# Performance work log

Hardware: AMD Instinct MI355X
Metric: run time of the kernel (lower is better)

## Reference

```python
import jax, jax.numpy as jnp
import numpy as np

N, IN_DIM, EMB = 65536, 768, 128
CB_SIZES = [8, 64, 512]
COMMIT = 0.25  # standard EMA-VQ commitment cost


def setup_inputs() -> dict:
    key = jax.random.key(0)
    ks = jax.random.split(key, 12)
    s = 0.02
    return {
        "x": jax.random.normal(ks[0], (N, IN_DIM), jnp.float32),
        "W_e1": jax.random.normal(ks[1], (IN_DIM, IN_DIM), jnp.float32) * s,
        "b_e1": jnp.zeros((IN_DIM,), jnp.float32),
        "W_e2": jax.random.normal(ks[2], (EMB, IN_DIM), jnp.float32) * s,
        "b_e2": jnp.zeros((EMB,), jnp.float32),
        "W_d1": jax.random.normal(ks[3], (EMB, EMB), jnp.float32) * s,
        "b_d1": jnp.zeros((EMB,), jnp.float32),
        "W_d2": jax.random.normal(ks[4], (EMB, EMB), jnp.float32) * s,
        "b_d2": jnp.zeros((EMB,), jnp.float32),
        "E0": jax.random.normal(ks[5], (CB_SIZES[0], EMB), jnp.float32),
        "E1": jax.random.normal(ks[6], (CB_SIZES[1], EMB), jnp.float32),
        "E2": jax.random.normal(ks[7], (CB_SIZES[2], EMB), jnp.float32),
    }


def _quantize(r, E):
    # squared L2 distances [N, K] = |r|^2 - 2 r.E^T + |E|^2
    d = (jnp.sum(r * r, axis=-1, keepdims=True)
         - 2.0 * jnp.einsum("nd,kd->nk", r, E)
         + jnp.sum(E * E, axis=-1))
    idx = jnp.argmin(d, axis=-1)          # [N]
    z_q = E[idx]                           # gather [N, EMB]
    loss = COMMIT * jnp.mean((jax.lax.stop_gradient(z_q) - r) ** 2)
    z_q_st = r + jax.lax.stop_gradient(z_q - r)  # straight-through
    return z_q_st, loss, idx


def reference(x, W_e1, b_e1, W_e2, b_e2, W_d1, b_d1, W_d2, b_d2, E0, E1, E2):
    # encoder MLP
    h = jax.nn.relu(x @ W_e1.T + b_e1)
    z = h @ W_e2.T + b_e2                 # [N, EMB]

    residual = z
    quantized_sum = jnp.zeros_like(z)
    total_loss = jnp.float32(0.0)
    all_indices = []
    for E in (E0, E1, E2):                # fixed depth=3 residual VQ loop
        z_q, loss, idx = _quantize(residual, E)
        residual = residual - z_q
        quantized_sum = quantized_sum + z_q
        total_loss = total_loss + loss
        all_indices.append(idx)

    # decoder MLP
    h2 = jax.nn.relu(quantized_sum @ W_d1.T + b_d1)
    reconstructed = h2 @ W_d2.T + b_d2    # [N, EMB]
    codes = jnp.stack(all_indices, axis=1)  # [N, depth]
    return reconstructed, total_loss, codes
```

## Files before the change

### kernel.cpp

```cpp
#include <hip/hip_runtime.h>

typedef _Float16 f16;
typedef __attribute__((ext_vector_type(4))) _Float16 f16x4;
typedef __attribute__((ext_vector_type(8))) _Float16 f16x8;
typedef __attribute__((ext_vector_type(4))) float    f32x4;

static constexpr int NROWS = 65536;
static constexpr int D_IN  = 768;
static constexpr int D_EMB = 128;
static constexpr long LOSS_OFF  = (long)NROWS * D_EMB;
static constexpr long CODES_OFF = LOSS_OFF + 1;

static constexpr long WOFF = 201326592L;
static constexpr long WE1H = 0,       WE1L = 589824;
static constexpr long WE2H = 1179648, WE2L = 1277952;
static constexpr long WD1F = 1376256, WD2F = 1392640;
static constexpr long PARTIAL_B = WOFF + 4194304L;

__device__ __forceinline__ float dot4(float4 a, float4 b){
  return fmaf(a.x,b.x, fmaf(a.y,b.y, fmaf(a.z,b.z, a.w*b.w)));
}

__device__ __forceinline__ void split4(float4 v, f16x4& hi, f16x4& lo){
  _Float16 h0=(_Float16)v.x, h1=(_Float16)v.y, h2=(_Float16)v.z, h3=(_Float16)v.w;
  hi[0]=h0; hi[1]=h1; hi[2]=h2; hi[3]=h3;
  lo[0]=(_Float16)((v.x-(float)h0)*2048.0f);
  lo[1]=(_Float16)((v.y-(float)h1)*2048.0f);
  lo[2]=(_Float16)((v.z-(float)h2)*2048.0f);
  lo[3]=(_Float16)((v.w-(float)h3)*2048.0f);
}

__device__ __forceinline__ void split8_reg(const float* v, f16x8& hi, f16x8& lo){
#pragma unroll
  for (int i = 0; i < 8; i++){
    _Float16 h = (_Float16)v[i];
    hi[i] = h;
    lo[i] = (_Float16)((v[i]-(float)h)*2048.0f);
  }
}

__global__ __launch_bounds__(256)
void split_weights_kernel(const float* __restrict__ We1, const float* __restrict__ We2,
                          const float* __restrict__ Wd1, const float* __restrict__ Wd2,
                          f16* __restrict__ wp){
  int t = blockIdx.x*256 + threadIdx.x;
  if (t >= 180224) return;
  if (t < 147456){
    long o4 = t; float4 v = *(const float4*)(We1 + o4*4);
    f16x4 h4, l4; split4(v, h4, l4);
    *(f16x4*)(wp + WE1H + o4*4) = h4; *(f16x4*)(wp + WE1L + o4*4) = l4;
  } else if (t < 172032){
    long o4 = t - 147456; float4 v = *(const float4*)(We2 + o4*4);
    f16x4 h4, l4; split4(v, h4, l4);
    *(f16x4*)(wp + WE2H + o4*4) = h4; *(f16x4*)(wp + WE2L + o4*4) = l4;
  } else if (t < 176128){
    long o4 = t - 172032; float4 v = *(const float4*)(Wd1 + o4*4);
    f16x4 h4; h4[0]=(_Float16)v.x; h4[1]=(_Float16)v.y; h4[2]=(_Float16)v.z; h4[3]=(_Float16)v.w;
    *(f16x4*)(wp + WD1F + o4*4) = h4;
  } else {
    long o4 = t - 176128; float4 v = *(const float4*)(Wd2 + o4*4);
    f16x4 h4; h4[0]=(_Float16)v.x; h4[1]=(_Float16)v.y; h4[2]=(_Float16)v.z; h4[3]=(_Float16)v.w;
    *(f16x4*)(wp + WD2F + o4*4) = h4;
  }
}

template<bool RELU>
__global__ __launch_bounds__(256, 2)
void gemm_mfma_kernel(const float* __restrict__ A, const float* __restrict__ B,
                      const float* __restrict__ bias, float* __restrict__ C,
                      int M, int N, int K) {
  constexpr int RS = 40;
  __shared__ f16 Ah[128*RS];
  __shared__ f16 Al[128*RS];
  __shared__ f16 Bhs[128*RS];
  __shared__ f16 Bls[128*RS];

  const int tid  = threadIdx.x;
  const int wave = tid >> 6, lane = tid & 63;
  const int wm = wave >> 1, wn = wave & 1;
  const int lr = lane & 15, lg = lane >> 4;
  const long m0 = (long)blockIdx.y * 128;
  const long n0 = (long)blockIdx.x * 128;
  const float* Ab = A + m0 * K;
  const float* Bb = B + n0 * K;
  const int srow = tid >> 3;
  const int sc4  = tid & 7;

  float4 pa[4], pb[4];
#pragma unroll
  for (int p = 0; p < 4; p++){
    pa[p] = *(const float4*)(Ab + (long)(p*32 + srow)*K + sc4*4);
    pb[p] = *(const float4*)(Bb + (long)(p*32 + srow)*K + sc4*4);
  }

  f32x4 accm[4][4], accc[4][4];
#pragma unroll
  for (int i = 0; i < 4; i++)
#pragma unroll
    for (int j = 0; j < 4; j++){
      accm[i][j] = (f32x4){0.f,0.f,0.f,0.f};
      accc[i][j] = (f32x4){0.f,0.f,0.f,0.f};
    }

  const int nt = K / 32;
  for (int t = 0; t < nt; t++){
    __syncthreads();
#pragma unroll
    for (int p = 0; p < 4; p++){
      int r = p*32 + srow;
      f16x4 h4, l4;
      split4(pa[p], h4, l4);
      *(f16x4*)&Ah[r*RS + sc4*4] = h4;
      *(f16x4*)&Al[r*RS + sc4*4] = l4;
      split4(pb[p], h4, l4);
      *(f16x4*)&Bhs[r*RS + sc4*4] = h4;
      *(f16x4*)&Bls[r*RS + sc4*4] = l4;
    }
    __syncthreads();
    if (t + 1 < nt){
      const float* An = Ab + (t+1)*32;
      const float* Bn = Bb + (t+1)*32;
#pragma unroll
      for (int p = 0; p < 4; p++){
        pa[p] = *(const float4*)(An + (long)(p*32 + srow)*K + sc4*4);
        pb[p] = *(const float4*)(Bn + (long)(p*32 + srow)*K + sc4*4);
      }
    }
    f16x8 ah[4], al[4];
#pragma unroll
    for (int mi = 0; mi < 4; mi++){
      int row = wm*64 + mi*16 + lr;
      ah[mi] = *(const f16x8*)&Ah[row*RS + lg*8];
      al[mi] = *(const f16x8*)&Al[row*RS + lg*8];
    }
#pragma unroll
    for (int ni = 0; ni < 4; ni++){
      int col = wn*64 + ni*16 + lr;
      f16x8 bh = *(const f16x8*)&Bhs[col*RS + lg*8];
      f16x8 bl = *(const f16x8*)&Bls[col*RS + lg*8];
#pragma unroll
      for (int mi = 0; mi < 4; mi++){
        accm[mi][ni] = __builtin_amdgcn_mfma_f32_16x16x32_f16(ah[mi], bh, accm[mi][ni], 0, 0, 0);
        accc[mi][ni] = __builtin_amdgcn_mfma_f32_16x16x32_f16(ah[mi], bl, accc[mi][ni], 0, 0, 0);
        accc[mi][ni] = __builtin_amdgcn_mfma_f32_16x16x32_f16(al[mi], bh, accc[mi][ni], 0, 0, 0);
      }
    }
  }

  float bv[4];
#pragma unroll
  for (int ni = 0; ni < 4; ni++) bv[ni] = bias[n0 + wn*64 + ni*16 + lr];
#pragma unroll
  for (int mi = 0; mi < 4; mi++){
#pragma unroll
    for (int ni = 0; ni < 4; ni++){
#pragma unroll
      for (int r = 0; r < 4; r++){
        float v = accm[mi][ni][r] + accc[mi][ni][r]*(1.0f/2048.0f) + bv[ni];
        if (RELU) v = fmaxf(v, 0.f);
        long row = m0 + wm*64 + mi*16 + lg*4 + r;
        C[row*N + n0 + wn*64 + ni*16 + lr] = v;
      }
    }
  }
}

template<bool RELU, bool OUT16>
__global__ __launch_bounds__(256)
void gemm_f16_dec(const f16* __restrict__ Ag, const f16* __restrict__ Bg,
                  const float* __restrict__ bias,
                  float* __restrict__ C32, f16* __restrict__ C16, int M){
  constexpr int RS = 136;
  __shared__ f16 As[128*RS];
  __shared__ f16 Bs[128*RS];
  const int tid = threadIdx.x;
  const int wave = tid >> 6, lane = tid & 63;
  const int wm = wave >> 1, wn = wave & 1;
  const int lr = lane & 15, lg = lane >> 4;
  const long m0 = (long)blockIdx.y * 128;
  const int srow = tid >> 1, sco = (tid & 1) * 64;

#pragma unroll
  for (int c = 0; c < 8; c++){
    *(f16x8*)&As[srow*RS + sco + c*8] = *(const f16x8*)(Ag + (m0+srow)*128 + sco + c*8);
    *(f16x8*)&Bs[srow*RS + sco + c*8] = *(const f16x8*)(Bg + (long)srow*128 + sco + c*8);
  }
  __syncthreads();

  f32x4 acc[4][4];
#pragma unroll
  for (int i = 0; i < 4; i++)
#pragma unroll
    for (int j = 0; j < 4; j++) acc[i][j] = (f32x4){0.f,0.f,0.f,0.f};

#pragma unroll
  for (int ks = 0; ks < 4; ks++){
    f16x8 a[4];
#pragma unroll
    for (int mi = 0; mi < 4; mi++)
      a[mi] = *(const f16x8*)&As[(wm*64 + mi*16 + lr)*RS + ks*32 + lg*8];
#pragma unroll
    for (int ni = 0; ni < 4; ni++){
      f16x8 b = *(const f16x8*)&Bs[(wn*64 + ni*16 + lr)*RS + ks*32 + lg*8];
#pragma unroll
      for (int mi = 0; mi < 4; mi++)
        acc[mi][ni] = __builtin_amdgcn_mfma_f32_16x16x32_f16(a[mi], b, acc[mi][ni], 0, 0, 0);
    }
  }

  float bv[4];
#pragma unroll
  for (int ni = 0; ni < 4; ni++) bv[ni] = bias[wn*64 + ni*16 + lr];
#pragma unroll
  for (int mi = 0; mi < 4; mi++){
#pragma unroll
    for (int ni = 0; ni < 4; ni++){
#pragma unroll
      for (int r = 0; r < 4; r++){
        float v = acc[mi][ni][r] + bv[ni];
        if (RELU) v = fmaxf(v, 0.f);
        long row = m0 + wm*64 + mi*16 + lg*4 + r;
        long col = wn*64 + ni*16 + lr;
        if (OUT16) C16[row*128 + col] = (_Float16)v;
        else       C32[row*128 + col] = v;
      }
    }
  }
}

__global__ __launch_bounds__(256)
void vq_mfma_kernel(const float* __restrict__ z,
                    const float* __restrict__ E0c, const float* __restrict__ E1c,
                    const float* __restrict__ E2c,
                    f16* __restrict__ q16, float* __restrict__ out,
                    float* __restrict__ partial){
  constexpr int VS = 132;
  constexpr int ES = 136;
  __shared__ float rs[64*VS];
  __shared__ f16 Eh[64*ES];
  __shared__ f16 El[64*ES];
  __shared__ float pE[4*64];
  __shared__ int   besti[3*64];
  __shared__ float wsum[4];

  const int tid  = threadIdx.x;
  const int wave = tid >> 6, lane = tid & 63;
  const int lr = lane & 15, lg = lane >> 4;
  const int row0 = blockIdx.x * 64;
  const int urow = tid & 63, uq = tid >> 6;
  const int sc = tid & 63, sq = tid >> 6;

#pragma unroll
  for (int i = 0; i < 8; i++){
    int idx = i*256 + tid;
    int r = idx >> 5, c = (idx & 31) * 4;
    *(float4*)&rs[r*VS + c] = *(const float4*)&z[(long)(row0 + r)*D_EMB + c];
  }

  float4 qa[8];
#pragma unroll
  for (int j = 0; j < 8; j++) qa[j] = make_float4(0.f,0.f,0.f,0.f);
  float lsum = 0.f;

  const float* Etab[3] = {E0c, E1c, E2c};
  const int    Ktab[3] = {8, 64, 512};

  for (int l = 0; l < 3; l++){
    const float* E = Etab[l];
    const int K = Ktab[l];

    __syncthreads();
    f16x8 ah[4], al[4];
#pragma unroll
    for (int ks = 0; ks < 4; ks++){
      float av[8];
      *(float4*)&av[0] = *(const float4*)&rs[(wave*16 + lr)*VS + ks*32 + lg*8];
      *(float4*)&av[4] = *(const float4*)&rs[(wave*16 + lr)*VS + ks*32 + lg*8 + 4];
      split8_reg(av, ah[ks], al[ks]);
    }

    float bd[4]; int bi[4];
#pragma unroll
    for (int r = 0; r < 4; r++){ bd[r] = 3.0e38f; bi[r] = 0x7fffffff; }

    for (int kbase = 0; kbase < K; kbase += 64){
      const int cn = (K - kbase < 64) ? (K - kbase) : 64;
      __syncthreads();
      if (sc < cn){
        float s = 0.f;
#pragma unroll
        for (int j = 0; j < 8; j++){
          float4 v = *(const float4*)&E[(long)(kbase + sc)*D_EMB + sq*32 + j*4];
          s += dot4(v, v);
          f16x4 h4, l4; split4(v, h4, l4);
          *(f16x4*)&Eh[sc*ES + sq*32 + j*4] = h4;
          *(f16x4*)&El[sc*ES + sq*32 + j*4] = l4;
        }
        pE[sq*64 + sc] = s;
      } else {
        f16x4 zz; zz[0]=(_Float16)0.f; zz[1]=(_Float16)0.f; zz[2]=(_Float16)0.f; zz[3]=(_Float16)0.f;
#pragma unroll
        for (int j = 0; j < 8; j++){
          *(f16x4*)&Eh[sc*ES + sq*32 + j*4] = zz;
          *(f16x4*)&El[sc*ES + sq*32 + j*4] = zz;
        }
        pE[sq*64 + sc] = 3.0e38f;
      }
      __syncthreads();

      const int cgmax = (cn + 15) >> 4;
      for (int cg = 0; cg < cgmax; cg++){
        f32x4 Sm = (f32x4){0.f,0.f,0.f,0.f};
        f32x4 Sc = (f32x4){0.f,0.f,0.f,0.f};
#pragma unroll
        for (int ks = 0; ks < 4; ks++){
          f16x8 bh = *(const f16x8*)&Eh[(cg*16 + lr)*ES + ks*32 + lg*8];
          f16x8 bl = *(const f16x8*)&El[(cg*16 + lr)*ES + ks*32 + lg*8];
          Sm = __builtin_amdgcn_mfma_f32_16x16x32_f16(ah[ks], bh, Sm, 0, 0, 0);
          Sc = __builtin_amdgcn_mfma_f32_16x16x32_f16(ah[ks], bl, Sc, 0, 0, 0);
          Sc = __builtin_amdgcn_mfma_f32_16x16x32_f16(al[ks], bh, Sc, 0, 0, 0);
        }
        int code = cg*16 + lr;
        float ne = pE[code] + pE[64+code] + pE[128+code] + pE[192+code];
        int kg = kbase + code;
#pragma unroll
        for (int r = 0; r < 4; r++){
          float S  = fmaf(Sc[r], 1.0f/2048.0f, Sm[r]);
          float sd = fmaf(-2.0f, S, ne);
          if (sd < bd[r]){ bd[r] = sd; bi[r] = kg; }
        }
      }
    }

#pragma unroll
    for (int r = 0; r < 4; r++){
#pragma unroll
      for (int off = 1; off < 16; off <<= 1){
        float ob = __shfl_xor(bd[r], off, 16);
        int   oi = __shfl_xor(bi[r], off, 16);
        if (ob < bd[r] || (ob == bd[r] && oi < bi[r])){ bd[r] = ob; bi[r] = oi; }
      }
      if (lr == 0) besti[l*64 + wave*16 + lg*4 + r] = bi[r];
    }
    __syncthreads();

    {
      int k = besti[l*64 + urow];
      const float* Er = E + (long)k*D_EMB + uq*32;
#pragma unroll
      for (int j = 0; j < 8; j++){
        float4 e = *(const float4*)&Er[j*4];
        float* rp = &rs[urow*VS + uq*32 + j*4];
        float4 r = *(const float4*)rp;
        float4 df = make_float4(e.x-r.x, e.y-r.y, e.z-r.z, e.w-r.w);
        lsum += dot4(df, df);
        *(float4*)rp = make_float4(r.x-e.x, r.y-e.y, r.z-e.z, r.w-e.w);
        qa[j].x += e.x; qa[j].y += e.y; qa[j].z += e.z; qa[j].w += e.w;
      }
    }
  }

  __syncthreads();
#pragma unroll
  for (int j = 0; j < 8; j++)
    *(float4*)&rs[urow*VS + uq*32 + j*4] = qa[j];
  __syncthreads();
#pragma unroll
  for (int i = 0; i < 8; i++){
    int idx = i*256 + tid;
    int r = idx >> 5, c = (idx & 31) * 4;
    float4 v = *(const float4*)&rs[r*VS + c];
    f16x4 h4; h4[0]=(_Float16)v.x; h4[1]=(_Float16)v.y; h4[2]=(_Float16)v.z; h4[3]=(_Float16)v.w;
    *(f16x4*)&q16[(long)(row0 + r)*D_EMB + c] = h4;
  }
  if (tid < 64){
    long n = row0 + tid;
    for (int l = 0; l < 3; l++)
      out[CODES_OFF + n*3 + l] = (float)besti[l*64 + tid];
  }
  for (int off = 32; off > 0; off >>= 1) lsum += __shfl_down(lsum, off);
  if ((tid & 63) == 0) wsum[tid >> 6] = lsum;
  __syncthreads();
  if (tid == 0) partial[blockIdx.x] = wsum[0] + wsum[1] + wsum[2] + wsum[3];
}

__global__ __launch_bounds__(256)
void loss_reduce_kernel(const float* __restrict__ partial, float* __restrict__ out){
  __shared__ float ws2[4];
  int tid = threadIdx.x;
  float s = 0.f;
  for (int i = tid; i < 1024; i += 256) s += partial[i];
  for (int off = 32; off > 0; off >>= 1) s += __shfl_down(s, off);
  if ((tid & 63) == 0) ws2[tid >> 6] = s;
  __syncthreads();
  if (tid == 0)
    out[LOSS_OFF] = (ws2[0] + ws2[1] + ws2[2] + ws2[3]) * (0.25f / (float)((long)NROWS * D_EMB));
}

extern "C" void kernel_launch(void* const* d_in, const int* in_sizes, int n_in,
                              void* d_out, int out_size, void* d_ws, size_t ws_size,
                              hipStream_t stream) {
  (void)in_sizes; (void)n_in; (void)out_size; (void)ws_size;
  const float* x   = (const float*)d_in[0];
  const float* We1 = (const float*)d_in[1];
  const float* be1 = (const float*)d_in[2];
  const float* We2 = (const float*)d_in[3];
  const float* be2 = (const float*)d_in[4];
  const float* Wd1 = (const float*)d_in[5];
  const float* bd1 = (const float*)d_in[6];
  const float* Wd2 = (const float*)d_in[7];
  const float* bd2 = (const float*)d_in[8];
  const float* E0  = (const float*)d_in[9];
  const float* E1  = (const float*)d_in[10];
  const float* E2  = (const float*)d_in[11];
  float* out = (float*)d_out;
  char*  ws  = (char*)d_ws;

  float* h    = (float*)ws;
  f16*   q16  = (f16*)ws;
  f16*   h216 = (f16*)(ws + 33554432L);
  f16*   wp   = (f16*)(ws + WOFF);
  float* partial = (float*)(ws + PARTIAL_B);
  float* z = out;

  dim3 blk(256);
  split_weights_kernel<<<dim3(704), blk, 0, stream>>>(We1, We2, Wd1, Wd2, wp);
  gemm_mfma_kernel<true ><<<dim3(D_IN/128,  NROWS/128), blk, 0, stream>>>(x, We1, be1, h, NROWS, D_IN,  D_IN);
  gemm_mfma_kernel<false><<<dim3(D_EMB/128, NROWS/128), blk, 0, stream>>>(h, We2, be2, z, NROWS, D_EMB, D_IN);
  vq_mfma_kernel<<<dim3(NROWS/64), blk, 0, stream>>>(z, E0, E1, E2, q16, out, partial);
  loss_reduce_kernel<<<dim3(1), blk, 0, stream>>>(partial, out);
  gemm_f16_dec<true, true ><<<dim3(1, NROWS/128), blk, 0, stream>>>(q16,  wp+WD1F, bd1, nullptr, h216, NROWS);
  gemm_f16_dec<false,false><<<dim3(1, NROWS/128), blk, 0, stream>>>(h216, wp+WD2F, bd2, out, nullptr, NROWS);
}
```

Measured before the change: 516.7 us.

## Load pre-split MFMA-packed encoder weights directly from global, skip B LDS staging

The encoder weight matrices are now split into f16 hi/lo once and stored in an MFMA-fragment-packed layout, so the encoder GEMMs read B operands straight from global/L2 into registers instead of re-splitting fp32 weights into LDS every tile. This removes per-tile B conversion work and halves LDS usage, which may raise occupancy. A block-index swizzle is also added to group workgroups for better L2 locality. The risk is added global-load latency on the B path, since it is no longer prefetched a tile ahead.

```diff
diff --git a/kernel.cpp b/kernel.cpp
--- a/kernel.cpp
+++ b/kernel.cpp
@@ -12,10 +12,10 @@
 static constexpr long CODES_OFF = LOSS_OFF + 1;
 
 static constexpr long WOFF = 201326592L;
-static constexpr long WE1H = 0,       WE1L = 589824;
-static constexpr long WE2H = 1179648, WE2L = 1277952;
+static constexpr long PK1H = 0,       PK1L = 589824;
+static constexpr long PK2H = 1179648, PK2L = 1277952;
 static constexpr long WD1F = 1376256, WD2F = 1392640;
-static constexpr long PARTIAL_B = WOFF + 4194304L;
+static constexpr long PARTIAL_B = WOFF + 3145728L;
 
 __device__ __forceinline__ float dot4(float4 a, float4 b){
   return fmaf(a.x,b.x, fmaf(a.y,b.y, fmaf(a.z,b.z, a.w*b.w)));
@@ -46,13 +46,20 @@
   int t = blockIdx.x*256 + threadIdx.x;
   if (t >= 180224) return;
   if (t < 147456){
-    long o4 = t; float4 v = *(const float4*)(We1 + o4*4);
+    int n = t / 192, k0 = (t % 192) * 4;
+    float4 v = *(const float4*)(We1 + (long)n*768 + k0);
     f16x4 h4, l4; split4(v, h4, l4);
-    *(f16x4*)(wp + WE1H + o4*4) = h4; *(f16x4*)(wp + WE1L + o4*4) = l4;
+    long idx = (((long)(n>>4)*24 + (k0>>5))*64 + ((k0>>3)&3)*16 + (n&15))*8 + (k0&7);
+    *(f16x4*)(wp + PK1H + idx) = h4;
+    *(f16x4*)(wp + PK1L + idx) = l4;
   } else if (t < 172032){
-    long o4 = t - 147456; float4 v = *(const float4*)(We2 + o4*4);
+    int u = t - 147456;
+    int n = u / 192, k0 = (u % 192) * 4;
+    float4 v = *(const float4*)(We2 + (long)n*768 + k0);
     f16x4 h4, l4; split4(v, h4, l4);
-    *(f16x4*)(wp + WE2H + o4*4) = h4; *(f16x4*)(wp + WE2L + o4*4) = l4;
+    long idx = (((long)(n>>4)*24 + (k0>>5))*64 + ((k0>>3)&3)*16 + (n&15))*8 + (k0&7);
+    *(f16x4*)(wp + PK2H + idx) = h4;
+    *(f16x4*)(wp + PK2L + idx) = l4;
   } else if (t < 176128){
     long o4 = t - 172032; float4 v = *(const float4*)(Wd1 + o4*4);
     f16x4 h4; h4[0]=(_Float16)v.x; h4[1]=(_Float16)v.y; h4[2]=(_Float16)v.z; h4[3]=(_Float16)v.w;
@@ -66,32 +73,35 @@
 
 template<bool RELU>
 __global__ __launch_bounds__(256, 2)
-void gemm_mfma_kernel(const float* __restrict__ A, const float* __restrict__ B,
-                      const float* __restrict__ bias, float* __restrict__ C,
-                      int M, int N, int K) {
+void gemm_bL2_kernel(const float* __restrict__ A,
+                     const f16* __restrict__ Bph, const f16* __restrict__ Bpl,
+                     const float* __restrict__ bias, float* __restrict__ C,
+                     int M, int N, int K){
   constexpr int RS = 40;
   __shared__ f16 Ah[128*RS];
   __shared__ f16 Al[128*RS];
-  __shared__ f16 Bhs[128*RS];
-  __shared__ f16 Bls[128*RS];
-
-  const int tid  = threadIdx.x;
+
+  const int tid = threadIdx.x;
   const int wave = tid >> 6, lane = tid & 63;
   const int wm = wave >> 1, wn = wave & 1;
   const int lr = lane & 15, lg = lane >> 4;
-  const long m0 = (long)blockIdx.y * 128;
-  const long n0 = (long)blockIdx.x * 128;
+
+  const int nwg = gridDim.x * gridDim.y;
+  const int lid = blockIdx.y * gridDim.x + blockIdx.x;
+  const int sw  = (lid & 7) * (nwg >> 3) + (lid >> 3);
+  const int bx  = sw % gridDim.x, by = sw / gridDim.x;
+
+  const long m0 = (long)by * 128;
+  const long n0 = (long)bx * 128;
+  const int kcs = K >> 5;
   const float* Ab = A + m0 * K;
-  const float* Bb = B + n0 * K;
-  const int srow = tid >> 3;
-  const int sc4  = tid & 7;
-
-  float4 pa[4], pb[4];
-#pragma unroll
-  for (int p = 0; p < 4; p++){
+  const int srow = tid >> 3, sc4 = tid & 7;
+  const int cb = (int)(n0 >> 4) + wn*4;
+
+  float4 pa[4];
+#pragma unroll
+  for (int p = 0; p < 4; p++)
     pa[p] = *(const float4*)(Ab + (long)(p*32 + srow)*K + sc4*4);
-    pb[p] = *(const float4*)(Bb + (long)(p*32 + srow)*K + sc4*4);
-  }
 
   f32x4 accm[4][4], accc[4][4];
 #pragma unroll
@@ -102,30 +112,32 @@
       accc[i][j] = (f32x4){0.f,0.f,0.f,0.f};
     }
 
-  const int nt = K / 32;
-  for (int t = 0; t < nt; t++){
+  for (int t = 0; t < kcs; t++){
     __syncthreads();
 #pragma unroll
     for (int p = 0; p < 4; p++){
       int r = p*32 + srow;
-      f16x4 h4, l4;
-      split4(pa[p], h4, l4);
+      f16x4 h4, l4; split4(pa[p], h4, l4);
       *(f16x4*)&Ah[r*RS + sc4*4] = h4;
       *(f16x4*)&Al[r*RS + sc4*4] = l4;
-      split4(pb[p], h4, l4);
-      *(f16x4*)&Bhs[r*RS + sc4*4] = h4;
-      *(f16x4*)&Bls[r*RS + sc4*4] = l4;
     }
     __syncthreads();
-    if (t + 1 < nt){
+
+    f16x8 bh[4], bl[4];
+#pragma unroll
+    for (int ni = 0; ni < 4; ni++){
+      long bo = ((long)(cb + ni)*kcs + t)*512 + lane*8;
+      bh[ni] = *(const f16x8*)(Bph + bo);
+      bl[ni] = *(const f16x8*)(Bpl + bo);
+    }
+
+    if (t + 1 < kcs){
       const float* An = Ab + (t+1)*32;
-      const float* Bn = Bb + (t+1)*32;
-#pragma unroll
-      for (int p = 0; p < 4; p++){
+#pragma unroll
+      for (int p = 0; p < 4; p++)
         pa[p] = *(const float4*)(An + (long)(p*32 + srow)*K + sc4*4);
-        pb[p] = *(const float4*)(Bn + (long)(p*32 + srow)*K + sc4*4);
-      }
-    }
+    }
+
     f16x8 ah[4], al[4];
 #pragma unroll
     for (int mi = 0; mi < 4; mi++){
@@ -135,14 +147,11 @@
     }
 #pragma unroll
     for (int ni = 0; ni < 4; ni++){
-      int col = wn*64 + ni*16 + lr;
-      f16x8 bh = *(const f16x8*)&Bhs[col*RS + lg*8];
-      f16x8 bl = *(const f16x8*)&Bls[col*RS + lg*8];
 #pragma unroll
       for (int mi = 0; mi < 4; mi++){
-        accm[mi][ni] = __builtin_amdgcn_mfma_f32_16x16x32_f16(ah[mi], bh, accm[mi][ni], 0, 0, 0);
-        accc[mi][ni] = __builtin_amdgcn_mfma_f32_16x16x32_f16(ah[mi], bl, accc[mi][ni], 0, 0, 0);
-        accc[mi][ni] = __builtin_amdgcn_mfma_f32_16x16x32_f16(al[mi], bh, accc[mi][ni], 0, 0, 0);
+        accm[mi][ni] = __builtin_amdgcn_mfma_f32_16x16x32_f16(ah[mi], bh[ni], accm[mi][ni], 0, 0, 0);
+        accc[mi][ni] = __builtin_amdgcn_mfma_f32_16x16x32_f16(ah[mi], bl[ni], accc[mi][ni], 0, 0, 0);
+        accc[mi][ni] = __builtin_amdgcn_mfma_f32_16x16x32_f16(al[mi], bh[ni], accc[mi][ni], 0, 0, 0);
       }
     }
   }
@@ -425,8 +434,10 @@
 
   dim3 blk(256);
   split_weights_kernel<<<dim3(704), blk, 0, stream>>>(We1, We2, Wd1, Wd2, wp);
-  gemm_mfma_kernel<true ><<<dim3(D_IN/128,  NROWS/128), blk, 0, stream>>>(x, We1, be1, h, NROWS, D_IN,  D_IN);
-  gemm_mfma_kernel<false><<<dim3(D_EMB/128, NROWS/128), blk, 0, stream>>>(h, We2, be2, z, NROWS, D_EMB, D_IN);
+  gemm_bL2_kernel<true ><<<dim3(D_IN/128,  NROWS/128), blk, 0, stream>>>(
+      x, wp+PK1H, wp+PK1L, be1, h, NROWS, D_IN,  D_IN);
+  gemm_bL2_kernel<false><<<dim3(D_EMB/128, NROWS/128), blk, 0, stream>>>(
+      h, wp+PK2H, wp+PK2L, be2, z, NROWS, D_EMB, D_IN);
   vq_mfma_kernel<<<dim3(NROWS/64), blk, 0, stream>>>(z, E0, E1, E2, q16, out, partial);
   loss_reduce_kernel<<<dim3(1), blk, 0, stream>>>(partial, out);
   gemm_f16_dec<true, true ><<<dim3(1, NROWS/128), blk, 0, stream>>>(q16,  wp+WD1F, bd1, nullptr, h216, NROWS);
```

After: 537.0 us. 1.04x slower.

## Double-buffer encoder GEMM LDS, use pre-split f16 weights, enlarge M tile

Applied to the files above, without the earlier changes.

The encoder GEMM now uses two LDS buffers, so the next K-slice is staged into one buffer while MFMAs run on the other, with one barrier per iteration instead of two. B operands are read from the weight hi/lo f16 split the earlier kernel already produces, rather than re-splitting the fp32 weights in every block. Blocks grow to 512 threads covering 256 rows, so each B tile is reused across more rows. The cost is twice the LDS (about 120KB per block with launch bounds asking for 2 blocks), which may cap occupancy.

```diff
diff --git a/kernel.cpp b/kernel.cpp
--- a/kernel.cpp
+++ b/kernel.cpp
@@ -65,33 +65,49 @@
 }
 
 template<bool RELU>
-__global__ __launch_bounds__(256, 2)
-void gemm_mfma_kernel(const float* __restrict__ A, const float* __restrict__ B,
-                      const float* __restrict__ bias, float* __restrict__ C,
-                      int M, int N, int K) {
+__global__ __launch_bounds__(512, 2)
+void gemm_v2_kernel(const float* __restrict__ A,
+                    const f16* __restrict__ Bhg, const f16* __restrict__ Blg,
+                    const float* __restrict__ bias, float* __restrict__ C,
+                    int M, int N, int K){
   constexpr int RS = 40;
-  __shared__ f16 Ah[128*RS];
-  __shared__ f16 Al[128*RS];
-  __shared__ f16 Bhs[128*RS];
-  __shared__ f16 Bls[128*RS];
-
-  const int tid  = threadIdx.x;
+  __shared__ f16 AhL[2][256*RS];
+  __shared__ f16 AlL[2][256*RS];
+  __shared__ f16 BhL[2][128*RS];
+  __shared__ f16 BlL[2][128*RS];
+
+  const int tid = threadIdx.x;
   const int wave = tid >> 6, lane = tid & 63;
   const int wm = wave >> 1, wn = wave & 1;
   const int lr = lane & 15, lg = lane >> 4;
-  const long m0 = (long)blockIdx.y * 128;
+  const long m0 = (long)blockIdx.y * 256;
   const long n0 = (long)blockIdx.x * 128;
-  const float* Ab = A + m0 * K;
-  const float* Bb = B + n0 * K;
-  const int srow = tid >> 3;
-  const int sc4  = tid & 7;
-
-  float4 pa[4], pb[4];
-#pragma unroll
-  for (int p = 0; p < 4; p++){
-    pa[p] = *(const float4*)(Ab + (long)(p*32 + srow)*K + sc4*4);
-    pb[p] = *(const float4*)(Bb + (long)(p*32 + srow)*K + sc4*4);
-  }
+
+  const int ar = tid >> 3;
+  const int ac = tid & 7;
+  const int br = tid >> 2;
+  const int bkc = tid & 3;
+
+  const int nt = K >> 5;
+
+  float4 pa[4];
+  f16x8 pbh, pbl;
+
+#pragma unroll
+  for (int i = 0; i < 4; i++)
+    pa[i] = *(const float4*)(A + (m0 + i*64 + ar)*K + ac*4);
+  pbh = *(const f16x8*)(Bhg + (n0 + br)*K + bkc*8);
+  pbl = *(const f16x8*)(Blg + (n0 + br)*K + bkc*8);
+
+#pragma unroll
+  for (int i = 0; i < 4; i++){
+    f16x4 h4, l4; split4(pa[i], h4, l4);
+    *(f16x4*)&AhL[0][(i*64 + ar)*RS + ac*4] = h4;
+    *(f16x4*)&AlL[0][(i*64 + ar)*RS + ac*4] = l4;
+  }
+  *(f16x8*)&BhL[0][br*RS + bkc*8] = pbh;
+  *(f16x8*)&BlL[0][br*RS + bkc*8] = pbl;
+  __syncthreads();
 
   f32x4 accm[4][4], accc[4][4];
 #pragma unroll
@@ -102,48 +118,50 @@
       accc[i][j] = (f32x4){0.f,0.f,0.f,0.f};
     }
 
-  const int nt = K / 32;
+  int cur = 0;
   for (int t = 0; t < nt; t++){
-    __syncthreads();
-#pragma unroll
-    for (int p = 0; p < 4; p++){
-      int r = p*32 + srow;
-      f16x4 h4, l4;
-      split4(pa[p], h4, l4);
-      *(f16x4*)&Ah[r*RS + sc4*4] = h4;
-      *(f16x4*)&Al[r*RS + sc4*4] = l4;
-      split4(pb[p], h4, l4);
-      *(f16x4*)&Bhs[r*RS + sc4*4] = h4;
-      *(f16x4*)&Bls[r*RS + sc4*4] = l4;
-    }
-    __syncthreads();
-    if (t + 1 < nt){
-      const float* An = Ab + (t+1)*32;
-      const float* Bn = Bb + (t+1)*32;
-#pragma unroll
-      for (int p = 0; p < 4; p++){
-        pa[p] = *(const float4*)(An + (long)(p*32 + srow)*K + sc4*4);
-        pb[p] = *(const float4*)(Bn + (long)(p*32 + srow)*K + sc4*4);
-      }
-    }
+    const bool more = (t + 1 < nt);
+    if (more){
+      const long ko = (long)(t+1) * 32;
+#pragma unroll
+      for (int i = 0; i < 4; i++)
+        pa[i] = *(const float4*)(A + (m0 + i*64 + ar)*K + ko + ac*4);
+      pbh = *(const f16x8*)(Bhg + (n0 + br)*K + ko + bkc*8);
+      pbl = *(const f16x8*)(Blg + (n0 + br)*K + ko + bkc*8);
+    }
+
     f16x8 ah[4], al[4];
 #pragma unroll
     for (int mi = 0; mi < 4; mi++){
       int row = wm*64 + mi*16 + lr;
-      ah[mi] = *(const f16x8*)&Ah[row*RS + lg*8];
-      al[mi] = *(const f16x8*)&Al[row*RS + lg*8];
+      ah[mi] = *(const f16x8*)&AhL[cur][row*RS + lg*8];
+      al[mi] = *(const f16x8*)&AlL[cur][row*RS + lg*8];
     }
 #pragma unroll
     for (int ni = 0; ni < 4; ni++){
       int col = wn*64 + ni*16 + lr;
-      f16x8 bh = *(const f16x8*)&Bhs[col*RS + lg*8];
-      f16x8 bl = *(const f16x8*)&Bls[col*RS + lg*8];
+      f16x8 bh = *(const f16x8*)&BhL[cur][col*RS + lg*8];
+      f16x8 bl = *(const f16x8*)&BlL[cur][col*RS + lg*8];
 #pragma unroll
       for (int mi = 0; mi < 4; mi++){
         accm[mi][ni] = __builtin_amdgcn_mfma_f32_16x16x32_f16(ah[mi], bh, accm[mi][ni], 0, 0, 0);
         accc[mi][ni] = __builtin_amdgcn_mfma_f32_16x16x32_f16(ah[mi], bl, accc[mi][ni], 0, 0, 0);
         accc[mi][ni] = __builtin_amdgcn_mfma_f32_16x16x32_f16(al[mi], bh, accc[mi][ni], 0, 0, 0);
       }
+    }
+
+    if (more){
+      int nb = cur ^ 1;
+#pragma unroll
+      for (int i = 0; i < 4; i++){
+        f16x4 h4, l4; split4(pa[i], h4, l4);
+        *(f16x4*)&AhL[nb][(i*64 + ar)*RS + ac*4] = h4;
+        *(f16x4*)&AlL[nb][(i*64 + ar)*RS + ac*4] = l4;
+      }
+      *(f16x8*)&BhL[nb][br*RS + bkc*8] = pbh;
+      *(f16x8*)&BlL[nb][br*RS + bkc*8] = pbl;
+      __syncthreads();
+      cur = nb;
     }
   }
 
@@ -425,8 +443,10 @@
 
   dim3 blk(256);
   split_weights_kernel<<<dim3(704), blk, 0, stream>>>(We1, We2, Wd1, Wd2, wp);
-  gemm_mfma_kernel<true ><<<dim3(D_IN/128,  NROWS/128), blk, 0, stream>>>(x, We1, be1, h, NROWS, D_IN,  D_IN);
-  gemm_mfma_kernel<false><<<dim3(D_EMB/128, NROWS/128), blk, 0, stream>>>(h, We2, be2, z, NROWS, D_EMB, D_IN);
+  gemm_v2_kernel<true ><<<dim3(D_IN/128,  NROWS/256), dim3(512), 0, stream>>>(
+      x, wp+WE1H, wp+WE1L, be1, h, NROWS, D_IN,  D_IN);
+  gemm_v2_kernel<false><<<dim3(D_EMB/128, NROWS/256), dim3(512), 0, stream>>>(
+      h, wp+WE2H, wp+WE2L, be2, z, NROWS, D_EMB, D_IN);
   vq_mfma_kernel<<<dim3(NROWS/64), blk, 0, stream>>>(z, E0, E1, E2, q16, out, partial);
   loss_reduce_kernel<<<dim3(1), blk, 0, stream>>>(partial, out);
   gemm_f16_dec<true, true ><<<dim3(1, NROWS/128), blk, 0, stream>>>(q16,  wp+WD1F, bd1, nullptr, h216, NROWS);
```

New measurement: 513.3 us. Within noise of the previous version (-0.7%).
